# Kernel tuning notes

Measured on AMD Instinct MI355X. Metric: run time of the kernel, lower is better.

## Reference

```python
import jax, jax.numpy as jnp
import numpy as np

N_NODES = 50000
N_EDGES = 800000


def _inv_sqrt_deg(idx, n):
    deg = jax.ops.segment_sum(jnp.ones(idx.shape, jnp.float32), idx, num_segments=n)
    return jnp.where(deg > 0, deg ** -0.5, 0.0)


def graph_conv(x, W, b, src, dst, norm_src, norm_dst):
    # DGL GraphConv, norm='both': D_dst^{-1/2} A D_src^{-1/2} X W + b
    # Apply weight before aggregation (out_feats < in_feats in both layers).
    h = (x * norm_src[:, None]) @ W            # [N, out]
    m = h[src]                                  # gather per-edge messages [E, out]
    agg = jax.ops.segment_sum(m, dst, num_segments=x.shape[0])
    return agg * norm_dst[:, None] + b


def setup_inputs() -> dict:
    key = jax.random.key(0)
    ks = jax.random.split(key, 6)
    x = jax.random.normal(ks[0], (N_NODES, 512), jnp.float32)
    W1 = jax.random.normal(ks[1], (512, 128), jnp.float32) * (512 ** -0.5)
    b1 = jnp.zeros((128,), jnp.float32)
    W2 = jax.random.normal(ks[2], (128, 40), jnp.float32) * (128 ** -0.5)
    b2 = jnp.zeros((40,), jnp.float32)
    src = jax.random.randint(ks[3], (N_EDGES,), 0, N_NODES, jnp.int32)
    dst = jax.random.randint(ks[4], (N_EDGES,), 0, N_NODES, jnp.int32)
    return {"x": x, "W1": W1, "b1": b1, "W2": W2, "b2": b2, "src": src, "dst": dst}


def reference(x, W1, b1, W2, b2, src, dst):
    n = x.shape[0]
    norm_src = _inv_sqrt_deg(src, n)  # out-degree based src norm
    norm_dst = _inv_sqrt_deg(dst, n)  # in-degree based dst norm
    h = graph_conv(x, W1, b1, src, dst, norm_src, norm_dst)
    h = jax.nn.relu(h)
    h = graph_conv(h, W2, b2, src, dst, norm_src, norm_dst)
    return h
```

## Files before the change

### kernel.cpp

```cpp
#include <hip/hip_runtime.h>
#include <hip/hip_bf16.h>

#define F0 512
#define F1 128
#define F2 40

#define NRP 12800
#define G_SL 64

typedef __attribute__((ext_vector_type(8))) short bf16x8;
typedef __attribute__((ext_vector_type(4))) float f32x4;

__device__ inline ushort f2bf(float f) {
    union { float f; uint u; } v; v.f = f;
    uint u = v.u;
    uint r = u + 0x7fffu + ((u >> 16) & 1u);
    return (ushort)(r >> 16);
}

#define CVT2(dst, a, b) { __hip_bfloat162 _t2 = __float22bfloat162_rn(make_float2(a, b)); __builtin_memcpy(&dst, &_t2, 4); }

__global__ __launch_bounds__(1024)
void hist_kernel(const int* __restrict__ src, const int* __restrict__ dst,
                 ushort* __restrict__ Gsrc, ushort* __restrict__ Gdst,
                 const float* __restrict__ W1, ushort* __restrict__ Wt, int n, int E) {
    if (blockIdx.x < (F0 * F1) / 1024) {
        int idx = blockIdx.x * 1024 + threadIdx.x;
        int k = idx >> 7, nn = idx & 127;
        Wt[nn * F0 + k] = f2bf(W1[idx]);
    }
    __shared__ uint cs[NRP / 2];
    __shared__ uint cd[NRP / 2];
    const int p = blockIdx.x / G_SL;
    const int g = blockIdx.x % G_SL;
    const int base = p * NRP;
    for (int i = threadIdx.x; i < NRP / 2; i += 1024) { cs[i] = 0; cd[i] = 0; }
    __syncthreads();
    const int Epg = (E + G_SL - 1) / G_SL;
    const int e0 = g * Epg;
    const int e1 = min(E, e0 + Epg);
    for (int i = e0 + (int)threadIdx.x; i < e1; i += 1024) {
        int s = src[i], d = dst[i];
        unsigned so = (unsigned)(s - base);
        unsigned dd = (unsigned)(d - base);
        if (so < (unsigned)NRP) atomicAdd(&cs[so >> 1], 1u << ((so & 1) * 16));
        if (dd < (unsigned)NRP) atomicAdd(&cd[dd >> 1], 1u << ((dd & 1) * 16));
    }
    __syncthreads();
    const int lim = min(NRP, n - base);
    for (int i = threadIdx.x; i < lim; i += 1024) {
        uint pcs = cs[i >> 1], pcd = cd[i >> 1];
        int sh = (i & 1) * 16;
        Gsrc[(size_t)g * n + base + i] = (ushort)((pcs >> sh) & 0xffffu);
        Gdst[(size_t)g * n + base + i] = (ushort)((pcd >> sh) & 0xffffu);
    }
}

__global__ __launch_bounds__(256)
void scanA_kernel(const ushort* __restrict__ Gsrc, const ushort* __restrict__ Gdst,
                  float* __restrict__ norm_src, float* __restrict__ norm_dst,
                  int* __restrict__ row_off, int* __restrict__ bsum, int n) {
    __shared__ int sm[256];
    int i = blockIdx.x * 256 + threadIdx.x;
    int s = 0, d = 0;
    if (i < n) {
#pragma unroll
        for (int g = 0; g < G_SL; g++) {
            s += Gsrc[(size_t)g * n + i];
            d += Gdst[(size_t)g * n + i];
        }
        norm_src[i] = s > 0 ? rsqrtf((float)s) : 0.f;
        norm_dst[i] = d > 0 ? rsqrtf((float)d) : 0.f;
    }
    sm[threadIdx.x] = (i < n) ? d : 0;
    __syncthreads();
    for (int off = 1; off < 256; off <<= 1) {
        int t = (threadIdx.x >= (unsigned)off) ? sm[threadIdx.x - off] : 0;
        __syncthreads();
        sm[threadIdx.x] += t;
        __syncthreads();
    }
    if (i < n) row_off[i + 1] = sm[threadIdx.x];
    if (threadIdx.x == 255) bsum[blockIdx.x] = sm[255];
}

__global__ __launch_bounds__(256)
void finalize_kernel(int* __restrict__ row_off, const int* __restrict__ bsum,
                     const ushort* __restrict__ Gdst, int* __restrict__ Goff, int n) {
    __shared__ int sm[256];
    const int b = blockIdx.x;
    const int t = threadIdx.x;
    sm[t] = (t < b) ? bsum[t] : 0;
    __syncthreads();
#pragma unroll
    for (int off = 128; off > 0; off >>= 1) {
        if (t < off) sm[t] += sm[t + off];
        __syncthreads();
    }
    const int excl = sm[0];
    const int v = b * 256 + t;
    if (v >= n) return;
    int raw = row_off[v];
    int start = excl + ((t == 0) ? 0 : raw);
    if (v == n - 1) {
        int rawn = row_off[n];
        row_off[n] = excl + rawn;
    }
    row_off[v] = start;
    int run = start;
#pragma unroll
    for (int g = 0; g < G_SL; g++) {
        size_t idx = (size_t)g * n + v;
        Goff[idx] = run;
        run += Gdst[idx];
    }
}

__global__ __launch_bounds__(1024)
void place_kernel(const int* __restrict__ src, const int* __restrict__ dst,
                  const int* __restrict__ Goff, int* __restrict__ edge_src, int n, int E) {
    __shared__ int cur[NRP];
    const int p = blockIdx.x / G_SL;
    const int g = blockIdx.x % G_SL;
    const int base = p * NRP;
    const int lim = min(NRP, n - base);
    for (int i = threadIdx.x; i < lim; i += 1024)
        cur[i] = Goff[(size_t)g * n + base + i];
    __syncthreads();
    const int Epg = (E + G_SL - 1) / G_SL;
    const int e0 = g * Epg;
    const int e1 = min(E, e0 + Epg);
    for (int i = e0 + (int)threadIdx.x; i < e1; i += 1024) {
        int d = dst[i];
        unsigned dd = (unsigned)(d - base);
        if (dd < (unsigned)lim) {
            int pos = atomicAdd(&cur[dd], 1);
            edge_src[pos] = src[i];
        }
    }
}

#define BM 64

#define LOADX(dst, k0) { dst = arok ? *reinterpret_cast<const float4*>(xptr + (k0)) : make_float4(0.f, 0.f, 0.f, 0.f); }

#define STAGE(buf, xv) {                                                        \
    uint _h0, _h1;                                                              \
    CVT2(_h0, xv.x, xv.y); CVT2(_h1, xv.z, xv.w);                               \
    *reinterpret_cast<uint2*>(&Al[buf][smi][sflane][shalf * 4]) = make_uint2(_h0, _h1); }

#define LOADB(k0, b) { b = *reinterpret_cast<const bf16x8*>(bp + (k0)); }

#define COMPUTE(buf, b) {                                                               \
    bf16x8 _a0 = *reinterpret_cast<const bf16x8*>(&Al[buf][0][lane][0]);                \
    bf16x8 _a1 = *reinterpret_cast<const bf16x8*>(&Al[buf][1][lane][0]);                \
    bf16x8 _a2 = *reinterpret_cast<const bf16x8*>(&Al[buf][2][lane][0]);                \
    bf16x8 _a3 = *reinterpret_cast<const bf16x8*>(&Al[buf][3][lane][0]);                \
    acc[0] = __builtin_amdgcn_mfma_f32_16x16x32_bf16(_a0, b, acc[0], 0, 0, 0);          \
    acc[1] = __builtin_amdgcn_mfma_f32_16x16x32_bf16(_a1, b, acc[1], 0, 0, 0);          \
    acc[2] = __builtin_amdgcn_mfma_f32_16x16x32_bf16(_a2, b, acc[2], 0, 0, 0);          \
    acc[3] = __builtin_amdgcn_mfma_f32_16x16x32_bf16(_a3, b, acc[3], 0, 0, 0); }

__global__ __launch_bounds__(512)
void gemm1_mfma(const float* __restrict__ x, const ushort* __restrict__ Wt,
                const float* __restrict__ norm_src, ushort* __restrict__ h1g, int n) {
    __shared__ __align__(16) ushort Al[2][4][64][8];

    const int tid = threadIdx.x;
    const int lane = tid & 63;
    const int w = tid >> 6;
    const int l15 = lane & 15;
    const int lq = lane >> 4;
    const int bm = blockIdx.x * BM;

    const int smi = tid >> 7;
    const int sflane = (tid >> 1) & 63;
    const int shalf = tid & 1;
    const int srow = smi * 16 + (sflane & 15);
    const int skc = ((sflane >> 4) << 3) + shalf * 4;
    const int grow = bm + srow;
    const bool arok = grow < n;
    const float* xptr = x + (size_t)(arok ? grow : 0) * F0 + skc;

    const ushort* bp = Wt + (size_t)(w * 16 + l15) * F0 + lq * 8;

    f32x4 acc[4] = {};
    float4 xnxt;
    bf16x8 bcur, bnxt;

    LOADX(xnxt, 0);
    LOADB(0, bcur);
    STAGE(0, xnxt);
    __syncthreads();

    for (int kt2 = 0; kt2 < 8; kt2++) {
        const int kb = kt2 * 2;
        {
            LOADX(xnxt, (kb + 1) * 32);
            LOADB((kb + 1) * 32, bnxt);
            COMPUTE(0, bcur);
            STAGE(1, xnxt);
            bcur = bnxt;
            __syncthreads();
        }
        if (kb + 1 < 15) {
            LOADX(xnxt, (kb + 2) * 32);
            LOADB((kb + 2) * 32, bnxt);
            COMPUTE(1, bcur);
            STAGE(0, xnxt);
            bcur = bnxt;
            __syncthreads();
        } else {
            COMPUTE(1, bcur);
        }
    }

#pragma unroll
    for (int mi = 0; mi < 4; mi++) {
        int rbase = bm + mi * 16 + lq * 4;
#pragma unroll
        for (int r = 0; r < 4; r++) {
            int row = rbase + r;
            if (row < n) {
                float ns = norm_src[row];
                h1g[(size_t)row * F1 + w * 16 + l15] = f2bf(acc[mi][r] * ns);
            }
        }
    }
}

__global__ __launch_bounds__(256)
void agg1_kernel(const ushort* __restrict__ h1g, const int* __restrict__ row_off,
                 const int* __restrict__ edge_src, const float* __restrict__ norm_dst,
                 const float* __restrict__ b1, ushort* __restrict__ h1, int n) {
    int wid = (blockIdx.x * blockDim.x + threadIdx.x) >> 6;
    int lane = threadIdx.x & 63;
    if (wid >= n) return;
    int beg = row_off[wid], end = row_off[wid + 1];
    float a0 = 0.f, a1 = 0.f;
    int e = beg;
    for (; e + 7 < end; e += 8) {
        int s[8];
#pragma unroll
        for (int j = 0; j < 8; j++) s[j] = edge_src[e + j];
        uint v[8];
#pragma unroll
        for (int j = 0; j < 8; j++)
            v[j] = *reinterpret_cast<const uint*>(&h1g[(size_t)s[j] * F1 + lane * 2]);
#pragma unroll
        for (int j = 0; j < 8; j++) {
            a0 += __uint_as_float(v[j] << 16);
            a1 += __uint_as_float(v[j] & 0xffff0000u);
        }
    }
    for (; e < end; ++e) {
        int s = edge_src[e];
        uint v = *reinterpret_cast<const uint*>(&h1g[(size_t)s * F1 + lane * 2]);
        a0 += __uint_as_float(v << 16);
        a1 += __uint_as_float(v & 0xffff0000u);
    }
    float nd = norm_dst[wid];
    float o0 = fmaxf(a0 * nd + b1[lane * 2 + 0], 0.f);
    float o1 = fmaxf(a1 * nd + b1[lane * 2 + 1], 0.f);
    __hip_bfloat162 p2 = __float22bfloat162_rn(make_float2(o0, o1));
    uint pu; __builtin_memcpy(&pu, &p2, 4);
    *reinterpret_cast<uint*>(&h1[(size_t)wid * F1 + lane * 2]) = pu;
}

__global__ __launch_bounds__(256)
void gemm2_kernel(const ushort* __restrict__ h1, const float* __restrict__ W2,
                  const float* __restrict__ norm_src, ushort* __restrict__ h2g, int n) {
    __shared__ __align__(16) float W2s[F1][F2];
    for (int i = threadIdx.x; i < F1 * F2; i += 256)
        W2s[i / F2][i % F2] = W2[i];
    __syncthreads();
    int node = blockIdx.x * 256 + threadIdx.x;
    if (node >= n) return;
    float nrm = norm_src[node];
    f32x4 acc4[10] = {};
    const ushort* row = &h1[(size_t)node * F1];
    for (int kc = 0; kc < 16; kc++) {
        uint4 u = *reinterpret_cast<const uint4*>(&row[kc * 8]);
        uint uu[4] = {u.x, u.y, u.z, u.w};
        float f[8];
#pragma unroll
        for (int i = 0; i < 4; i++) {
            f[2 * i + 0] = __uint_as_float(uu[i] << 16);
            f[2 * i + 1] = __uint_as_float(uu[i] & 0xffff0000u);
        }
#pragma unroll
        for (int j = 0; j < 8; j++) {
#pragma unroll
            for (int c4 = 0; c4 < 10; c4++) {
                f32x4 wv = *reinterpret_cast<const f32x4*>(&W2s[kc * 8 + j][c4 * 4]);
                acc4[c4] += f[j] * wv;
            }
        }
    }
    ushort* orow = &h2g[(size_t)node * F2];
#pragma unroll
    for (int c4 = 0; c4 < 10; c4++) {
        f32x4 o = acc4[c4] * nrm;
        __hip_bfloat162 pa = __float22bfloat162_rn(make_float2(o[0], o[1]));
        __hip_bfloat162 pb = __float22bfloat162_rn(make_float2(o[2], o[3]));
        uint2 pk;
        __builtin_memcpy(&pk.x, &pa, 4);
        __builtin_memcpy(&pk.y, &pb, 4);
        *reinterpret_cast<uint2*>(&orow[c4 * 4]) = pk;
    }
}

__global__ __launch_bounds__(256)
void agg2_kernel(const ushort* __restrict__ h2g, const int* __restrict__ row_off,
                 const int* __restrict__ edge_src, const float* __restrict__ norm_dst,
                 const float* __restrict__ b2, float* __restrict__ out, int n) {
    int wid = (blockIdx.x * blockDim.x + threadIdx.x) >> 6;
    int lane = threadIdx.x & 63;
    if (wid >= n) return;
    int beg = row_off[wid], end = row_off[wid + 1];
    float a0 = 0.f, a1 = 0.f;
    int e = beg;
    const bool act = lane < 20;
    for (; e + 7 < end; e += 8) {
        int s[8];
#pragma unroll
        for (int j = 0; j < 8; j++) s[j] = edge_src[e + j];
        if (act) {
            uint v[8];
#pragma unroll
            for (int j = 0; j < 8; j++)
                v[j] = *reinterpret_cast<const uint*>(&h2g[(size_t)s[j] * F2 + lane * 2]);
#pragma unroll
            for (int j = 0; j < 8; j++) {
                a0 += __uint_as_float(v[j] << 16);
                a1 += __uint_as_float(v[j] & 0xffff0000u);
            }
        }
    }
    for (; e < end; ++e) {
        int s = edge_src[e];
        if (act) {
            uint v = *reinterpret_cast<const uint*>(&h2g[(size_t)s * F2 + lane * 2]);
            a0 += __uint_as_float(v << 16);
            a1 += __uint_as_float(v & 0xffff0000u);
        }
    }
    if (act) {
        float nd = norm_dst[wid];
        float o0 = a0 * nd + b2[lane * 2 + 0];
        float o1 = a1 * nd + b2[lane * 2 + 1];
        *reinterpret_cast<float2*>(&out[(size_t)wid * F2 + lane * 2]) = make_float2(o0, o1);
    }
}

extern "C" void kernel_launch(void* const* d_in, const int* in_sizes, int n_in,
                              void* d_out, int out_size, void* d_ws, size_t ws_size,
                              hipStream_t stream) {
    const float* x  = (const float*)d_in[0];
    const float* W1 = (const float*)d_in[1];
    const float* b1 = (const float*)d_in[2];
    const float* W2 = (const float*)d_in[3];
    const float* b2 = (const float*)d_in[4];
    const int* src  = (const int*)d_in[5];
    const int* dst  = (const int*)d_in[6];
    float* out = (float*)d_out;

    const int n = in_sizes[0] / F0;
    const int E = in_sizes[5];
    const int nb = (n + 255) / 256;
    const int P = (n + NRP - 1) / NRP;

    char* ws = (char*)d_ws;
    auto alloc = [&](size_t bytes) -> char* {
        char* p = ws;
        ws += (bytes + 255) & ~(size_t)255;
        return p;
    };
    int* row_off   = (int*)alloc((size_t)(n + 1) * 4);
    int* bsum      = (int*)alloc(256 * 4);
    int* edge_srcs = (int*)alloc((size_t)E * 4);
    float* norm_src_d = (float*)alloc((size_t)n * 4);
    float* norm_dst_d = (float*)alloc((size_t)n * 4);
    ushort* W1t = (ushort*)alloc((size_t)F1 * F0 * 2);
    ushort* h1g = (ushort*)alloc((size_t)n * F1 * 2);
    ushort* h1  = (ushort*)alloc((size_t)n * F1 * 2);
    ushort* h2g = h1g;

    ushort* Gsrc = (ushort*)h1g;
    ushort* Gdst = Gsrc + (size_t)G_SL * n;
    int* Goff = (int*)h1;

    hist_kernel<<<P * G_SL, 1024, 0, stream>>>(src, dst, Gsrc, Gdst, W1, W1t, n, E);
    scanA_kernel<<<nb, 256, 0, stream>>>(Gsrc, Gdst, norm_src_d, norm_dst_d, row_off, bsum, n);
    finalize_kernel<<<nb, 256, 0, stream>>>(row_off, bsum, Gdst, Goff, n);
    place_kernel<<<P * G_SL, 1024, 0, stream>>>(src, dst, Goff, edge_srcs, n, E);
    gemm1_mfma<<<(n + BM - 1) / BM, 512, 0, stream>>>(x, W1t, norm_src_d, h1g, n);
    agg1_kernel<<<(n + 3) / 4, 256, 0, stream>>>(h1g, row_off, edge_srcs, norm_dst_d, b1, h1, n);
    gemm2_kernel<<<(n + 255) / 256, 256, 0, stream>>>(h1, W2, norm_src_d, h2g, n);
    agg2_kernel<<<(n + 3) / 4, 256, 0, stream>>>(h2g, row_off, edge_srcs, norm_dst_d, b2, out, n);
}
```

Before: 181.9 us.

## Stage larger K tiles of x in swizzled LDS to cut barriers in gemm1

The first-layer GEMM now loads 128-wide K slices of x per stage with four float4 loads per thread, where it used to load 32-wide slices. Each slice is converted to bf16 and stored in a 16KB double-buffered LDS tile using an XOR swizzle to avoid bank conflicts. This cuts the number of __syncthreads from 16 to 4 and coalesces global reads along full rows. In exchange it uses more LDS and more registers per thread, and the longer stages may hide less latency between barriers.

```diff
diff --git a/kernel.cpp b/kernel.cpp
--- a/kernel.cpp
+++ b/kernel.cpp
@@ -142,29 +142,38 @@
 
 #define BM 64
 
-#define LOADX(dst, k0) { dst = arok ? *reinterpret_cast<const float4*>(xptr + (k0)) : make_float4(0.f, 0.f, 0.f, 0.f); }
-
-#define STAGE(buf, xv) {                                                        \
-    uint _h0, _h1;                                                              \
-    CVT2(_h0, xv.x, xv.y); CVT2(_h1, xv.z, xv.w);                               \
-    *reinterpret_cast<uint2*>(&Al[buf][smi][sflane][shalf * 4]) = make_uint2(_h0, _h1); }
+#define LOADT(f, i, kto) {                                                             \
+    int _r = (i) * 16 + (tid >> 5);                                                    \
+    f = (bm + _r < n) ? *reinterpret_cast<const float4*>(                              \
+            x + (size_t)(bm + _r) * F0 + (kto) * 128 + (tid & 31) * 4)                 \
+                      : make_float4(0.f, 0.f, 0.f, 0.f); }
+
+#define STAGEW(bufp, i, f) {                                                           \
+    int _r = (i) * 16 + (tid >> 5);                                                    \
+    int _c4 = tid & 31;                                                                \
+    uint _h0, _h1;                                                                     \
+    CVT2(_h0, f.x, f.y); CVT2(_h1, f.z, f.w);                                          \
+    int _byte = _r * 256 + ((((_c4) >> 1) ^ (_r & 7)) << 4) + ((_c4 & 1) << 3);        \
+    *reinterpret_cast<uint2*>((bufp) + _byte) = make_uint2(_h0, _h1); }
 
 #define LOADB(k0, b) { b = *reinterpret_cast<const bf16x8*>(bp + (k0)); }
 
-#define COMPUTE(buf, b) {                                                               \
-    bf16x8 _a0 = *reinterpret_cast<const bf16x8*>(&Al[buf][0][lane][0]);                \
-    bf16x8 _a1 = *reinterpret_cast<const bf16x8*>(&Al[buf][1][lane][0]);                \
-    bf16x8 _a2 = *reinterpret_cast<const bf16x8*>(&Al[buf][2][lane][0]);                \
-    bf16x8 _a3 = *reinterpret_cast<const bf16x8*>(&Al[buf][3][lane][0]);                \
-    acc[0] = __builtin_amdgcn_mfma_f32_16x16x32_bf16(_a0, b, acc[0], 0, 0, 0);          \
-    acc[1] = __builtin_amdgcn_mfma_f32_16x16x32_bf16(_a1, b, acc[1], 0, 0, 0);          \
-    acc[2] = __builtin_amdgcn_mfma_f32_16x16x32_bf16(_a2, b, acc[2], 0, 0, 0);          \
+#define COMPUTE(bufp, kt2, b) {                                                        \
+    const int _cx = ((((kt2) * 4) + lq) ^ (l15 & 7)) << 4;                             \
+    const char* _pb = (bufp) + l15 * 256 + _cx;                                        \
+    bf16x8 _a0 = *reinterpret_cast<const bf16x8*>(_pb + 0 * 4096);                     \
+    bf16x8 _a1 = *reinterpret_cast<const bf16x8*>(_pb + 1 * 4096);                     \
+    bf16x8 _a2 = *reinterpret_cast<const bf16x8*>(_pb + 2 * 4096);                     \
+    bf16x8 _a3 = *reinterpret_cast<const bf16x8*>(_pb + 3 * 4096);                     \
+    acc[0] = __builtin_amdgcn_mfma_f32_16x16x32_bf16(_a0, b, acc[0], 0, 0, 0);         \
+    acc[1] = __builtin_amdgcn_mfma_f32_16x16x32_bf16(_a1, b, acc[1], 0, 0, 0);         \
+    acc[2] = __builtin_amdgcn_mfma_f32_16x16x32_bf16(_a2, b, acc[2], 0, 0, 0);         \
     acc[3] = __builtin_amdgcn_mfma_f32_16x16x32_bf16(_a3, b, acc[3], 0, 0, 0); }
 
 __global__ __launch_bounds__(512)
 void gemm1_mfma(const float* __restrict__ x, const ushort* __restrict__ Wt,
                 const float* __restrict__ norm_src, ushort* __restrict__ h1g, int n) {
-    __shared__ __align__(16) ushort Al[2][4][64][8];
+    __shared__ __align__(16) char Al[2][16384];
 
     const int tid = threadIdx.x;
     const int lane = tid & 63;
@@ -172,46 +181,40 @@
     const int l15 = lane & 15;
     const int lq = lane >> 4;
     const int bm = blockIdx.x * BM;
-
-    const int smi = tid >> 7;
-    const int sflane = (tid >> 1) & 63;
-    const int shalf = tid & 1;
-    const int srow = smi * 16 + (sflane & 15);
-    const int skc = ((sflane >> 4) << 3) + shalf * 4;
-    const int grow = bm + srow;
-    const bool arok = grow < n;
-    const float* xptr = x + (size_t)(arok ? grow : 0) * F0 + skc;
+    (void)lane;
 
     const ushort* bp = Wt + (size_t)(w * 16 + l15) * F0 + lq * 8;
 
     f32x4 acc[4] = {};
-    float4 xnxt;
+    float4 f0, f1, f2, f3;
     bf16x8 bcur, bnxt;
 
-    LOADX(xnxt, 0);
     LOADB(0, bcur);
-    STAGE(0, xnxt);
-    __syncthreads();
-
-    for (int kt2 = 0; kt2 < 8; kt2++) {
-        const int kb = kt2 * 2;
-        {
-            LOADX(xnxt, (kb + 1) * 32);
-            LOADB((kb + 1) * 32, bnxt);
-            COMPUTE(0, bcur);
-            STAGE(1, xnxt);
+    LOADT(f0, 0, 0); LOADT(f1, 1, 0); LOADT(f2, 2, 0); LOADT(f3, 3, 0);
+    STAGEW(&Al[0][0], 0, f0); STAGEW(&Al[0][0], 1, f1);
+    STAGEW(&Al[0][0], 2, f2); STAGEW(&Al[0][0], 3, f3);
+    __syncthreads();
+
+    for (int kto = 0; kto < 4; ++kto) {
+        const int cb = kto & 1;
+        char* bufp = &Al[cb][0];
+        if (kto < 3) {
+            LOADT(f0, 0, kto + 1); LOADT(f1, 1, kto + 1);
+            LOADT(f2, 2, kto + 1); LOADT(f3, 3, kto + 1);
+        }
+#pragma unroll
+        for (int kt2 = 0; kt2 < 4; ++kt2) {
+            const int kg = kto * 4 + kt2;
+            const int knxt = (kg + 1 < 16) ? (kg + 1) : 15;
+            LOADB(knxt * 32, bnxt);
+            COMPUTE(bufp, kt2, bcur);
             bcur = bnxt;
+        }
+        if (kto < 3) {
+            char* nbufp = &Al[cb ^ 1][0];
+            STAGEW(nbufp, 0, f0); STAGEW(nbufp, 1, f1);
+            STAGEW(nbufp, 2, f2); STAGEW(nbufp, 3, f3);
             __syncthreads();
-        }
-        if (kb + 1 < 15) {
-            LOADX(xnxt, (kb + 2) * 32);
-            LOADB((kb + 2) * 32, bnxt);
-            COMPUTE(1, bcur);
-            STAGE(0, xnxt);
-            bcur = bnxt;
-            __syncthreads();
-        } else {
-            COMPUTE(1, bcur);
         }
     }
 
```

Measured after the change: 187.3 us. 1.03x slower.
